# Kernel optimization log

Measured on AMD Instinct MI355X. Metric: run time of the kernel, lower is better.

## Reference

```python
import jax, jax.numpy as jnp
import numpy as np

K = 1024  # codebook size
D = 256   # code dim
B, L = 32, 1024  # batch, tokens


def setup_inputs() -> dict:
    key = jax.random.key(0)
    k1, k2 = jax.random.split(key)
    z_e_x = jax.random.normal(k1, (B, L, D), dtype=jnp.float32)
    # nn.Embedding weight init: uniform(-1/K, 1/K)
    embedding = jax.random.uniform(k2, (K, D), dtype=jnp.float32,
                                   minval=-1.0 / K, maxval=1.0 / K)
    return {"z_e_x": z_e_x, "embedding": embedding}


def reference(z_e_x, embedding):
    # vq(): nearest-neighbor codebook lookup -> integer indices, shape z_e_x.shape[:-1]
    flat = z_e_x.reshape(-1, z_e_x.shape[-1])                      # [N, D]
    # squared L2 distances via expansion: ||z||^2 - 2 z.e + ||e||^2
    d = (jnp.sum(flat * flat, axis=1, keepdims=True)
         - 2.0 * flat @ embedding.T
         + jnp.sum(embedding * embedding, axis=1))                 # [N, K]
    idx = jnp.argmin(d, axis=1)                                    # [N]
    return idx.reshape(z_e_x.shape[:-1])
```

## Files before the change

### kernel.cpp

```cpp
#include <hip/hip_runtime.h>


#define DDIM 256
#define KCODES 1024
#define TAU 1.6e-4f
#define WIN 1.2e-4f
#define LISTCAP 16384
#define CANDCAP 16
#define P2GRID 2048

typedef __attribute__((ext_vector_type(8))) _Float16 f16x8;
typedef __attribute__((ext_vector_type(2))) _Float16 h2;
typedef __attribute__((ext_vector_type(4))) float f32x4;
typedef __attribute__((ext_vector_type(8))) unsigned short u16x8;

__device__ __forceinline__ float block128_sq(const float* __restrict__ a)
{
#pragma clang fp contract(off)
    float r[8];
    #pragma unroll
    for (int j = 0; j < 8; ++j) { float v = a[j]; r[j] = v * v; }
    #pragma unroll
    for (int i = 8; i < 128; i += 8) {
        #pragma unroll
        for (int j = 0; j < 8; ++j) { float v = a[i + j]; r[j] = r[j] + v * v; }
    }
    return ((r[0] + r[1]) + (r[2] + r[3])) + ((r[4] + r[5]) + (r[6] + r[7]));
}

__global__ __launch_bounds__(256) void vq_prep(
    const float* __restrict__ emb, unsigned short* __restrict__ e16,
    float* __restrict__ s2, int* __restrict__ count)
{
    const int tid = threadIdx.x;
    if (blockIdx.x == 0 && tid == 0) *count = 0;

    const int id = blockIdx.x * 256 + tid;
    const float* src = emb + (size_t)id * 8;
    float4 p0 = *reinterpret_cast<const float4*>(src);
    float4 p1 = *reinterpret_cast<const float4*>(src + 4);
    float fv[8] = {p0.x, p0.y, p0.z, p0.w, p1.x, p1.y, p1.z, p1.w};
    u16x8 vh;
    #pragma unroll
    for (int e = 0; e < 8; ++e) {
        _Float16 h = (_Float16)(fv[e] * 1024.0f);
        vh[e] = __builtin_bit_cast(unsigned short, h);
    }
    *reinterpret_cast<u16x8*>(e16 + (size_t)id * 8) = vh;

    if (tid < 8) {
        const int c = blockIdx.x * 8 + tid;
        const float* e = emb + (size_t)c * DDIM;
        s2[c] = block128_sq(e) + block128_sq(e + 128);
    }
}

__global__ __launch_bounds__(256, 2) void vq_pass1(
    const float* __restrict__ z, const unsigned short* __restrict__ e16,
    const float* __restrict__ s2g, int* __restrict__ out,
    int* __restrict__ count, int* __restrict__ list, int N)
{
    __shared__ __align__(16) unsigned short Bt[3][8192];
    __shared__ float s2s[KCODES];
    __shared__ float Lbv[2][64], Lsv[2][64];
    __shared__ int   Lbk[2][64];

    const int tid  = threadIdx.x;
    const int wid  = tid >> 6, lane = tid & 63;
    const int ll   = lane & 15, lg = lane >> 4;
    const int rowHalf  = wid & 1, codeHalf = wid >> 1;
    const int rowbase  = blockIdx.x * 64 + rowHalf * 32;
    const int chbase   = codeHalf * 512;

    for (int c = tid; c < KCODES; c += 256) s2s[c] = s2g[c];

    const int sB     = (ll >> 1) & 3;
    const int rdbase = ll * 32 + ((lg ^ sB) << 3);

    f16x8 afrag[8][2];
    #pragma unroll
    for (int ks = 0; ks < 8; ++ks)
        #pragma unroll
        for (int m = 0; m < 2; ++m) {
            const float* zp = z + (size_t)(rowbase + 16 * m + ll) * DDIM + ks * 32 + lg * 8;
            float4 p0 = *reinterpret_cast<const float4*>(zp);
            float4 p1 = *reinterpret_cast<const float4*>(zp + 4);
            float fv[8] = {p0.x, p0.y, p0.z, p0.w, p1.x, p1.y, p1.z, p1.w};
            #pragma unroll
            for (int e = 0; e < 8; ++e) afrag[ks][m][e] = (_Float16)fv[e];
        }

    #define STAGE(nt_, buf_)                                                      \
        {                                                                         \
            const int nt_v = (nt_);                                               \
            _Pragma("unroll")                                                     \
            for (int q = 0; q < 4; ++q) {                                         \
                int id = q * 256 + tid;                                           \
                int half = id >> 9, rem = id & 511, cl = rem >> 2, pc = rem & 3;  \
                int clog = pc ^ ((cl >> 1) & 3);                                  \
                const unsigned short* src = e16 +                                 \
                    (size_t)(half * 512 + (nt_v >> 3) * 128 + cl) * DDIM          \
                        + (nt_v & 7) * 32 + clog * 8;                             \
                __builtin_amdgcn_global_load_lds(                                 \
                    (const __attribute__((address_space(1))) void*)src,           \
                    (__attribute__((address_space(3))) void*)&Bt[buf_][(size_t)id * 8], \
                    16, 0, 0);                                                    \
            }                                                                     \
        }

    f32x4 acc[2][8];
    float bv[2][4], sv[2][4];
    int   bk[2][4];
    #pragma unroll
    for (int m = 0; m < 2; ++m)
        #pragma unroll
        for (int j = 0; j < 4; ++j) { bv[m][j] = 3.4e38f; sv[m][j] = 3.4e38f; bk[m][j] = 0; }

    STAGE(0, 0);
    STAGE(1, 1);

    for (int ct = 0; ct < 4; ++ct) {
        const f32x4 zero4 = {0.f, 0.f, 0.f, 0.f};
        #pragma unroll
        for (int m = 0; m < 2; ++m)
            #pragma unroll
            for (int n = 0; n < 8; ++n) acc[m][n] = zero4;

        #pragma unroll
        for (int ks = 0; ks < 8; ++ks) {
            const int t = ct * 8 + ks;
            if (t < 31) asm volatile("s_waitcnt vmcnt(4)" ::: "memory");
            else        asm volatile("s_waitcnt vmcnt(0)" ::: "memory");
            __builtin_amdgcn_s_barrier();
            __builtin_amdgcn_sched_barrier(0);

            const unsigned short* bbase = &Bt[t % 3][codeHalf * 4096];
            #pragma unroll
            for (int n = 0; n < 8; ++n) {
                f16x8 bh = *reinterpret_cast<const f16x8*>(bbase + n * 512 + rdbase);
                #pragma unroll
                for (int m = 0; m < 2; ++m)
                    acc[m][n] = __builtin_amdgcn_mfma_f32_16x16x32_f16(
                        afrag[ks][m], bh, acc[m][n], 0, 0, 0);
            }

            if (t + 2 < 32) STAGE(t + 2, (t + 2) % 3);
        }

        #pragma unroll
        for (int n = 0; n < 8; ++n) {
            const int c = chbase + ct * 128 + n * 16 + ll;
            const float s2v = s2s[c];
            #pragma unroll
            for (int m = 0; m < 2; ++m)
                #pragma unroll
                for (int j = 0; j < 4; ++j) {
                    float v = fmaf(-0.001953125f, acc[m][n][j], s2v);
                    if (v < bv[m][j] || (v == bv[m][j] && c < bk[m][j])) {
                        sv[m][j] = bv[m][j]; bv[m][j] = v; bk[m][j] = c;
                    } else {
                        sv[m][j] = fminf(sv[m][j], v);
                    }
                }
        }
    }
    #undef STAGE

    #pragma unroll
    for (int off = 1; off < 16; off <<= 1) {
        #pragma unroll
        for (int m = 0; m < 2; ++m)
            #pragma unroll
            for (int j = 0; j < 4; ++j) {
                float ob = __shfl_xor(bv[m][j], off, 64);
                int   ok = __shfl_xor(bk[m][j], off, 64);
                float os = __shfl_xor(sv[m][j], off, 64);
                if (ob < bv[m][j] || (ob == bv[m][j] && ok < bk[m][j])) {
                    sv[m][j] = fminf(bv[m][j], os); bv[m][j] = ob; bk[m][j] = ok;
                } else {
                    sv[m][j] = fminf(sv[m][j], ob);
                }
            }
    }

    if (ll == 0) {
        #pragma unroll
        for (int m = 0; m < 2; ++m)
            #pragma unroll
            for (int j = 0; j < 4; ++j) {
                int rib = rowHalf * 32 + 16 * m + lg * 4 + j;
                Lbv[codeHalf][rib] = bv[m][j];
                Lsv[codeHalf][rib] = sv[m][j];
                Lbk[codeHalf][rib] = bk[m][j];
            }
    }
    __syncthreads();

    if (tid < 64) {
        const int r = blockIdx.x * 64 + tid;
        if (r < N) {
            float b0 = Lbv[0][tid], s0 = Lsv[0][tid]; int k0 = Lbk[0][tid];
            float b1 = Lbv[1][tid], s1 = Lsv[1][tid]; int k1 = Lbk[1][tid];
            float bb, ss; int kk;
            if (b1 < b0) { bb = b1; kk = k1; ss = fminf(s1, b0); }
            else         { bb = b0; kk = k0; ss = fminf(s0, b1); }
            out[r] = kk;
            if (ss - bb <= TAU) {
                int pos = atomicAdd(count, 1);
                if (pos < LISTCAP) list[pos] = r;
            }
        }
    }
}

__global__ __launch_bounds__(256, 4) void vq_pass2(
    const float* __restrict__ z, const float* __restrict__ emb,
    const unsigned short* __restrict__ e16, const float* __restrict__ s2g,
    const int* __restrict__ count, const int* __restrict__ list,
    int* __restrict__ out)
{
#pragma clang fp contract(off)
    __shared__ __align__(16) float zls[DDIM];
    __shared__ float vls[KCODES];
    __shared__ float s2s[KCODES];
    __shared__ float s1sh, bvsh;
    __shared__ float wmin[4];
    __shared__ int   candc[CANDCAP];
    __shared__ float cand_v[CANDCAP];
    __shared__ int   ncand;

    const int tid  = threadIdx.x;
    const int wv   = tid >> 6, lane = tid & 63;
    const int cslot = lane >> 2;
    const int sub   = lane & 3;

    int cnt = *count; if (cnt > LISTCAP) cnt = LISTCAP;
    if ((int)blockIdx.x >= cnt) return;

    for (int c = tid; c < KCODES; c += 256) s2s[c] = s2g[c];

    for (int idx = blockIdx.x; idx < cnt; idx += P2GRID) {
        const int row = list[idx];

        if (tid < 64)
            *reinterpret_cast<float4*>(&zls[tid * 4]) =
                *reinterpret_cast<const float4*>(z + (size_t)row * DDIM + tid * 4);
        if (tid == 65) ncand = 0;
        __syncthreads();

        if (tid == 0) s1sh = block128_sq(zls) + block128_sq(zls + 128);

        h2 z16[32];
        {
            const float2* zp2 = reinterpret_cast<const float2*>(&zls[0]);
            #pragma unroll
            for (int q = 0; q < 8; ++q)
                #pragma unroll
                for (int j = 0; j < 4; ++j) {
                    float2 f = zp2[q * 16 + sub * 4 + j];
                    h2 a; a[0] = (_Float16)f.x; a[1] = (_Float16)f.y;
                    z16[q * 4 + j] = a;
                }
        }

        #pragma unroll 1
        for (int i = 0; i < 16; ++i) {
            const int c = wv * 256 + i * 16 + cslot;
            const unsigned short* base = e16 + (size_t)c * DDIM;

            float p = 0.f;
            #pragma unroll
            for (int h = 0; h < 2; ++h) {
                f16x8 e0 = *reinterpret_cast<const f16x8*>(base + (4 * h + 0) * 32 + sub * 8);
                f16x8 e1 = *reinterpret_cast<const f16x8*>(base + (4 * h + 1) * 32 + sub * 8);
                f16x8 e2 = *reinterpret_cast<const f16x8*>(base + (4 * h + 2) * 32 + sub * 8);
                f16x8 e3 = *reinterpret_cast<const f16x8*>(base + (4 * h + 3) * 32 + sub * 8);
                #pragma unroll
                for (int j = 0; j < 4; ++j) {
                    h2 a0; a0[0] = e0[2 * j]; a0[1] = e0[2 * j + 1];
                    h2 a1; a1[0] = e1[2 * j]; a1[1] = e1[2 * j + 1];
                    h2 a2; a2[0] = e2[2 * j]; a2[1] = e2[2 * j + 1];
                    h2 a3; a3[0] = e3[2 * j]; a3[1] = e3[2 * j + 1];
#if __has_builtin(__builtin_amdgcn_fdot2)
                    p = __builtin_amdgcn_fdot2(a0, z16[(4 * h + 0) * 4 + j], p, false);
                    p = __builtin_amdgcn_fdot2(a1, z16[(4 * h + 1) * 4 + j], p, false);
                    p = __builtin_amdgcn_fdot2(a2, z16[(4 * h + 2) * 4 + j], p, false);
                    p = __builtin_amdgcn_fdot2(a3, z16[(4 * h + 3) * 4 + j], p, false);
#else
                    p = fmaf((float)a0[0], (float)z16[(4 * h + 0) * 4 + j][0], p);
                    p = fmaf((float)a0[1], (float)z16[(4 * h + 0) * 4 + j][1], p);
                    p = fmaf((float)a1[0], (float)z16[(4 * h + 1) * 4 + j][0], p);
                    p = fmaf((float)a1[1], (float)z16[(4 * h + 1) * 4 + j][1], p);
                    p = fmaf((float)a2[0], (float)z16[(4 * h + 2) * 4 + j][0], p);
                    p = fmaf((float)a2[1], (float)z16[(4 * h + 2) * 4 + j][1], p);
                    p = fmaf((float)a3[0], (float)z16[(4 * h + 3) * 4 + j][0], p);
                    p = fmaf((float)a3[1], (float)z16[(4 * h + 3) * 4 + j][1], p);
#endif
                }
            }
            p += __shfl_xor(p, 1, 64);
            p += __shfl_xor(p, 2, 64);
            if (sub == 0)
                vls[c] = fmaf(-0.001953125f, p, s2s[c]);
        }
        __syncthreads();

        float m = 3.4e38f;
        #pragma unroll
        for (int k = 0; k < 4; ++k) m = fminf(m, vls[tid + 256 * k]);
        #pragma unroll
        for (int off = 1; off < 64; off <<= 1) m = fminf(m, __shfl_xor(m, off, 64));
        if (lane == 0) wmin[wv] = m;
        __syncthreads();
        if (tid == 0)
            bvsh = fminf(fminf(wmin[0], wmin[1]), fminf(wmin[2], wmin[3]));
        __syncthreads();

        const float thr = bvsh + WIN;
        #pragma unroll
        for (int k = 0; k < 4; ++k) {
            int c = tid + 256 * k;
            if (vls[c] <= thr) {
                int p = atomicAdd(&ncand, 1);
                if (p < CANDCAP) candc[p] = c;
            }
        }
        __syncthreads();
        int nc2 = ncand; if (nc2 > CANDCAP) nc2 = CANDCAP;
        const float s1 = s1sh;

        for (int i = wv; i < nc2; i += 4) {
            const int c = candc[i];
            float4 ev4 = *reinterpret_cast<const float4*>(emb + (size_t)c * DDIM + lane * 4);
            const float* zq = &zls[lane * 4];
            double ds = (double)zq[0] * (double)ev4.x;
            ds = fma((double)zq[1], (double)ev4.y, ds);
            ds = fma((double)zq[2], (double)ev4.z, ds);
            ds = fma((double)zq[3], (double)ev4.w, ds);
            #pragma unroll
            for (int off = 1; off < 64; off <<= 1)
                ds += __shfl_xor(ds, off, 64);
            if (lane == 0) {
                float twog = 2.0f * (float)ds;
                float t1   = s1 - twog;
                cand_v[i]  = t1 + s2s[c];
            }
        }
        __syncthreads();

        if (tid == 0) {
            float bb = 3.4e38f; int kb = KCODES - 1;
            for (int i = 0; i < nc2; ++i) {
                float dv = cand_v[i]; int c = candc[i];
                if (dv < bb || (dv == bb && c < kb)) { bb = dv; kb = c; }
            }
            out[row] = kb;
        }
        __syncthreads();
    }
}

extern "C" void kernel_launch(void* const* d_in, const int* in_sizes, int n_in,
                              void* d_out, int out_size, void* d_ws, size_t ws_size,
                              hipStream_t stream) {
    const float* z   = (const float*)d_in[0];
    const float* emb = (const float*)d_in[1];
    int*   out   = (int*)d_out;
    float* s2    = (float*)d_ws;
    int*   count = (int*)((char*)d_ws + 4096);
    int*   list  = (int*)((char*)d_ws + 4224);
    unsigned short* e16 = (unsigned short*)((char*)d_ws + 131072);
    const int N = in_sizes[0] / DDIM;

    vq_prep<<<dim3(128), dim3(256), 0, stream>>>(emb, e16, s2, count);
    vq_pass1<<<dim3(N / 64), dim3(256), 0, stream>>>(z, e16, s2, out, count, list, N);
    vq_pass2<<<dim3(P2GRID), dim3(256), 0, stream>>>(z, emb, e16, s2, count, list, out);
}
```

Before: 74.40 us.

## Restructure VQ pass1 to 128-row blocks with per-wave full-codebook sweep

Pass1 now uses 512-thread blocks covering 128 rows. Each wave owns 16 rows and scans all 1024 codes, instead of splitting code halves across waves and merging them through shared memory. The codebook is staged in 128-code chunks covering the full depth, double-buffered with one barrier per chunk instead of one per 32-wide K slice. This cuts barrier count and drops the cross-wave LDS merge, and each staged B tile is reused by 8 waves. The cost is a larger LDS footprint (128KB of staging), a full vmcnt(0) wait before each chunk, and half the A-fragment reuse per B read.

```diff
diff --git a/kernel.cpp b/kernel.cpp
--- a/kernel.cpp
+++ b/kernel.cpp
@@ -55,52 +55,45 @@
     }
 }
 
-__global__ __launch_bounds__(256, 2) void vq_pass1(
+__global__ __launch_bounds__(512, 2) void vq_pass1(
     const float* __restrict__ z, const unsigned short* __restrict__ e16,
     const float* __restrict__ s2g, int* __restrict__ out,
     int* __restrict__ count, int* __restrict__ list, int N)
 {
-    __shared__ __align__(16) unsigned short Bt[3][8192];
+    __shared__ __align__(16) unsigned short Bt[2][32768];
     __shared__ float s2s[KCODES];
-    __shared__ float Lbv[2][64], Lsv[2][64];
-    __shared__ int   Lbk[2][64];
 
     const int tid  = threadIdx.x;
     const int wid  = tid >> 6, lane = tid & 63;
     const int ll   = lane & 15, lg = lane >> 4;
-    const int rowHalf  = wid & 1, codeHalf = wid >> 1;
-    const int rowbase  = blockIdx.x * 64 + rowHalf * 32;
-    const int chbase   = codeHalf * 512;
-
-    for (int c = tid; c < KCODES; c += 256) s2s[c] = s2g[c];
+    const int rowbase = blockIdx.x * 128 + wid * 16;
+
+    for (int c = tid; c < KCODES; c += 512) s2s[c] = s2g[c];
 
     const int sB     = (ll >> 1) & 3;
     const int rdbase = ll * 32 + ((lg ^ sB) << 3);
 
-    f16x8 afrag[8][2];
-    #pragma unroll
-    for (int ks = 0; ks < 8; ++ks)
-        #pragma unroll
-        for (int m = 0; m < 2; ++m) {
-            const float* zp = z + (size_t)(rowbase + 16 * m + ll) * DDIM + ks * 32 + lg * 8;
-            float4 p0 = *reinterpret_cast<const float4*>(zp);
-            float4 p1 = *reinterpret_cast<const float4*>(zp + 4);
-            float fv[8] = {p0.x, p0.y, p0.z, p0.w, p1.x, p1.y, p1.z, p1.w};
-            #pragma unroll
-            for (int e = 0; e < 8; ++e) afrag[ks][m][e] = (_Float16)fv[e];
-        }
-
-    #define STAGE(nt_, buf_)                                                      \
+    f16x8 afrag[8];
+    #pragma unroll
+    for (int ks = 0; ks < 8; ++ks) {
+        const float* zp = z + (size_t)(rowbase + ll) * DDIM + ks * 32 + lg * 8;
+        float4 p0 = *reinterpret_cast<const float4*>(zp);
+        float4 p1 = *reinterpret_cast<const float4*>(zp + 4);
+        float fv[8] = {p0.x, p0.y, p0.z, p0.w, p1.x, p1.y, p1.z, p1.w};
+        #pragma unroll
+        for (int e = 0; e < 8; ++e) afrag[ks][e] = (_Float16)fv[e];
+    }
+
+    #define STAGE(ct_, buf_)                                                      \
         {                                                                         \
-            const int nt_v = (nt_);                                               \
+            const int ct_v = (ct_);                                               \
             _Pragma("unroll")                                                     \
-            for (int q = 0; q < 4; ++q) {                                         \
-                int id = q * 256 + tid;                                           \
-                int half = id >> 9, rem = id & 511, cl = rem >> 2, pc = rem & 3;  \
+            for (int q = 0; q < 8; ++q) {                                         \
+                int id = q * 512 + tid;                                           \
+                int ks = id >> 9, rem = id & 511, cl = rem >> 2, pc = rem & 3;    \
                 int clog = pc ^ ((cl >> 1) & 3);                                  \
                 const unsigned short* src = e16 +                                 \
-                    (size_t)(half * 512 + (nt_v >> 3) * 128 + cl) * DDIM          \
-                        + (nt_v & 7) * 32 + clog * 8;                             \
+                    (size_t)(ct_v * 128 + cl) * DDIM + ks * 32 + clog * 8;        \
                 __builtin_amdgcn_global_load_lds(                                 \
                     (const __attribute__((address_space(1))) void*)src,           \
                     (__attribute__((address_space(3))) void*)&Bt[buf_][(size_t)id * 8], \
@@ -108,60 +101,50 @@
             }                                                                     \
         }
 
-    f32x4 acc[2][8];
-    float bv[2][4], sv[2][4];
-    int   bk[2][4];
-    #pragma unroll
-    for (int m = 0; m < 2; ++m)
-        #pragma unroll
-        for (int j = 0; j < 4; ++j) { bv[m][j] = 3.4e38f; sv[m][j] = 3.4e38f; bk[m][j] = 0; }
+    float bv[4], sv[4];
+    int   bk[4];
+    #pragma unroll
+    for (int j = 0; j < 4; ++j) { bv[j] = 3.4e38f; sv[j] = 3.4e38f; bk[j] = 0; }
 
     STAGE(0, 0);
-    STAGE(1, 1);
-
-    for (int ct = 0; ct < 4; ++ct) {
+
+    for (int ct = 0; ct < 8; ++ct) {
+        const int buf = ct & 1;
+        asm volatile("s_waitcnt vmcnt(0)" ::: "memory");
+        __builtin_amdgcn_s_barrier();
+        __builtin_amdgcn_sched_barrier(0);
+
+        if (ct < 7) STAGE(ct + 1, buf ^ 1);
+
+        f32x4 acc[8];
         const f32x4 zero4 = {0.f, 0.f, 0.f, 0.f};
         #pragma unroll
-        for (int m = 0; m < 2; ++m)
-            #pragma unroll
-            for (int n = 0; n < 8; ++n) acc[m][n] = zero4;
+        for (int n = 0; n < 8; ++n) acc[n] = zero4;
 
         #pragma unroll
         for (int ks = 0; ks < 8; ++ks) {
-            const int t = ct * 8 + ks;
-            if (t < 31) asm volatile("s_waitcnt vmcnt(4)" ::: "memory");
-            else        asm volatile("s_waitcnt vmcnt(0)" ::: "memory");
-            __builtin_amdgcn_s_barrier();
-            __builtin_amdgcn_sched_barrier(0);
-
-            const unsigned short* bbase = &Bt[t % 3][codeHalf * 4096];
             #pragma unroll
             for (int n = 0; n < 8; ++n) {
-                f16x8 bh = *reinterpret_cast<const f16x8*>(bbase + n * 512 + rdbase);
-                #pragma unroll
-                for (int m = 0; m < 2; ++m)
-                    acc[m][n] = __builtin_amdgcn_mfma_f32_16x16x32_f16(
-                        afrag[ks][m], bh, acc[m][n], 0, 0, 0);
-            }
-
-            if (t + 2 < 32) STAGE(t + 2, (t + 2) % 3);
+                f16x8 bh = *reinterpret_cast<const f16x8*>(
+                    &Bt[buf][ks * 4096 + n * 512 + rdbase]);
+                acc[n] = __builtin_amdgcn_mfma_f32_16x16x32_f16(
+                    afrag[ks], bh, acc[n], 0, 0, 0);
+            }
         }
 
         #pragma unroll
         for (int n = 0; n < 8; ++n) {
-            const int c = chbase + ct * 128 + n * 16 + ll;
+            const int c = ct * 128 + n * 16 + ll;
             const float s2v = s2s[c];
             #pragma unroll
-            for (int m = 0; m < 2; ++m)
-                #pragma unroll
-                for (int j = 0; j < 4; ++j) {
-                    float v = fmaf(-0.001953125f, acc[m][n][j], s2v);
-                    if (v < bv[m][j] || (v == bv[m][j] && c < bk[m][j])) {
-                        sv[m][j] = bv[m][j]; bv[m][j] = v; bk[m][j] = c;
-                    } else {
-                        sv[m][j] = fminf(sv[m][j], v);
-                    }
+            for (int j = 0; j < 4; ++j) {
+                float v = fmaf(-0.001953125f, acc[n][j], s2v);
+                if (v < bv[j] || (v == bv[j] && c < bk[j])) {
+                    sv[j] = bv[j]; bv[j] = v; bk[j] = c;
+                } else {
+                    sv[j] = fminf(sv[j], v);
                 }
+            }
         }
     }
     #undef STAGE
@@ -169,45 +152,28 @@
     #pragma unroll
     for (int off = 1; off < 16; off <<= 1) {
         #pragma unroll
-        for (int m = 0; m < 2; ++m)
-            #pragma unroll
-            for (int j = 0; j < 4; ++j) {
-                float ob = __shfl_xor(bv[m][j], off, 64);
-                int   ok = __shfl_xor(bk[m][j], off, 64);
-                float os = __shfl_xor(sv[m][j], off, 64);
-                if (ob < bv[m][j] || (ob == bv[m][j] && ok < bk[m][j])) {
-                    sv[m][j] = fminf(bv[m][j], os); bv[m][j] = ob; bk[m][j] = ok;
-                } else {
-                    sv[m][j] = fminf(sv[m][j], ob);
+        for (int j = 0; j < 4; ++j) {
+            float ob = __shfl_xor(bv[j], off, 64);
+            int   ok = __shfl_xor(bk[j], off, 64);
+            float os = __shfl_xor(sv[j], off, 64);
+            if (ob < bv[j] || (ob == bv[j] && ok < bk[j])) {
+                sv[j] = fminf(bv[j], os); bv[j] = ob; bk[j] = ok;
+            } else {
+                sv[j] = fminf(sv[j], ob);
+            }
+        }
+    }
+
+    if (ll == 0) {
+        #pragma unroll
+        for (int j = 0; j < 4; ++j) {
+            int r = rowbase + lg * 4 + j;
+            if (r < N) {
+                out[r] = bk[j];
+                if (sv[j] - bv[j] <= TAU) {
+                    int pos = atomicAdd(count, 1);
+                    if (pos < LISTCAP) list[pos] = r;
                 }
-            }
-    }
-
-    if (ll == 0) {
-        #pragma unroll
-        for (int m = 0; m < 2; ++m)
-            #pragma unroll
-            for (int j = 0; j < 4; ++j) {
-                int rib = rowHalf * 32 + 16 * m + lg * 4 + j;
-                Lbv[codeHalf][rib] = bv[m][j];
-                Lsv[codeHalf][rib] = sv[m][j];
-                Lbk[codeHalf][rib] = bk[m][j];
-            }
-    }
-    __syncthreads();
-
-    if (tid < 64) {
-        const int r = blockIdx.x * 64 + tid;
-        if (r < N) {
-            float b0 = Lbv[0][tid], s0 = Lsv[0][tid]; int k0 = Lbk[0][tid];
-            float b1 = Lbv[1][tid], s1 = Lsv[1][tid]; int k1 = Lbk[1][tid];
-            float bb, ss; int kk;
-            if (b1 < b0) { bb = b1; kk = k1; ss = fminf(s1, b0); }
-            else         { bb = b0; kk = k0; ss = fminf(s0, b1); }
-            out[r] = kk;
-            if (ss - bb <= TAU) {
-                int pos = atomicAdd(count, 1);
-                if (pos < LISTCAP) list[pos] = r;
             }
         }
     }
@@ -373,6 +339,6 @@
     const int N = in_sizes[0] / DDIM;
 
     vq_prep<<<dim3(128), dim3(256), 0, stream>>>(emb, e16, s2, count);
-    vq_pass1<<<dim3(N / 64), dim3(256), 0, stream>>>(z, e16, s2, out, count, list, N);
+    vq_pass1<<<dim3(N / 128), dim3(512), 0, stream>>>(z, e16, s2, out, count, list, N);
     vq_pass2<<<dim3(P2GRID), dim3(256), 0, stream>>>(z, emb, e16, s2, count, list, out);
 }
```

After: 72.89 us. 2.0% less time.

## Process 128 rows per block with full-K code tiles and double buffering

Applied to the files above, without the earlier changes.

Pass1 now gives each wave 32 rows against all 1024 codes instead of splitting codes between wave pairs. Each stage loads a whole 128-code by 256-dim fp16 tile (64 KB per buffer, double-buffered), so there is one barrier per 128-code tile instead of one per k-slice. This also removes the cross-wave LDS merge of the two code halves. Codebook reuse per block doubles, but LDS use rises to about 132 KB, occupancy drops to one block per CU with half as many blocks, and the fetch of each tile is waited on fully before compute.

```diff
diff --git a/kernel.cpp b/kernel.cpp
--- a/kernel.cpp
+++ b/kernel.cpp
@@ -55,29 +55,44 @@
     }
 }
 
-__global__ __launch_bounds__(256, 2) void vq_pass1(
+__global__ __launch_bounds__(256, 1) void vq_pass1(
     const float* __restrict__ z, const unsigned short* __restrict__ e16,
     const float* __restrict__ s2g, int* __restrict__ out,
     int* __restrict__ count, int* __restrict__ list, int N)
 {
-    __shared__ __align__(16) unsigned short Bt[3][8192];
+    __shared__ __align__(16) unsigned short Bt[2][32768];
     __shared__ float s2s[KCODES];
-    __shared__ float Lbv[2][64], Lsv[2][64];
-    __shared__ int   Lbk[2][64];
 
     const int tid  = threadIdx.x;
     const int wid  = tid >> 6, lane = tid & 63;
     const int ll   = lane & 15, lg = lane >> 4;
-    const int rowHalf  = wid & 1, codeHalf = wid >> 1;
-    const int rowbase  = blockIdx.x * 64 + rowHalf * 32;
-    const int chbase   = codeHalf * 512;
-
-    for (int c = tid; c < KCODES; c += 256) s2s[c] = s2g[c];
+    const int rowbase = blockIdx.x * 128 + wid * 32;
 
     const int sB     = (ll >> 1) & 3;
     const int rdbase = ll * 32 + ((lg ^ sB) << 3);
 
-    f16x8 afrag[8][2];
+    #define STAGE(ct_, buf_)                                                      \
+        {                                                                         \
+            const int ct_v = (ct_);                                               \
+            _Pragma("unroll")                                                     \
+            for (int q = 0; q < 16; ++q) {                                        \
+                int id = q * 256 + tid;                                           \
+                int ks = id >> 9, rem = id & 511, cl = rem >> 2, pc = rem & 3;    \
+                int clog = pc ^ ((cl >> 1) & 3);                                  \
+                const unsigned short* src = e16 +                                 \
+                    (size_t)(ct_v * 128 + cl) * DDIM + ks * 32 + clog * 8;        \
+                __builtin_amdgcn_global_load_lds(                                 \
+                    (const __attribute__((address_space(1))) void*)src,           \
+                    (__attribute__((address_space(3))) void*)&Bt[buf_][(size_t)id * 8], \
+                    16, 0, 0);                                                    \
+            }                                                                     \
+        }
+
+    STAGE(0, 0);
+
+    for (int c = tid; c < KCODES; c += 256) s2s[c] = s2g[c];
+
+    f16x8 afrag[2][8];
     #pragma unroll
     for (int ks = 0; ks < 8; ++ks)
         #pragma unroll
@@ -87,28 +102,9 @@
             float4 p1 = *reinterpret_cast<const float4*>(zp + 4);
             float fv[8] = {p0.x, p0.y, p0.z, p0.w, p1.x, p1.y, p1.z, p1.w};
             #pragma unroll
-            for (int e = 0; e < 8; ++e) afrag[ks][m][e] = (_Float16)fv[e];
-        }
-
-    #define STAGE(nt_, buf_)                                                      \
-        {                                                                         \
-            const int nt_v = (nt_);                                               \
-            _Pragma("unroll")                                                     \
-            for (int q = 0; q < 4; ++q) {                                         \
-                int id = q * 256 + tid;                                           \
-                int half = id >> 9, rem = id & 511, cl = rem >> 2, pc = rem & 3;  \
-                int clog = pc ^ ((cl >> 1) & 3);                                  \
-                const unsigned short* src = e16 +                                 \
-                    (size_t)(half * 512 + (nt_v >> 3) * 128 + cl) * DDIM          \
-                        + (nt_v & 7) * 32 + clog * 8;                             \
-                __builtin_amdgcn_global_load_lds(                                 \
-                    (const __attribute__((address_space(1))) void*)src,           \
-                    (__attribute__((address_space(3))) void*)&Bt[buf_][(size_t)id * 8], \
-                    16, 0, 0);                                                    \
-            }                                                                     \
-        }
-
-    f32x4 acc[2][8];
+            for (int e = 0; e < 8; ++e) afrag[m][ks][e] = (_Float16)fv[e];
+        }
+
     float bv[2][4], sv[2][4];
     int   bk[2][4];
     #pragma unroll
@@ -116,10 +112,15 @@
         #pragma unroll
         for (int j = 0; j < 4; ++j) { bv[m][j] = 3.4e38f; sv[m][j] = 3.4e38f; bk[m][j] = 0; }
 
-    STAGE(0, 0);
-    STAGE(1, 1);
-
-    for (int ct = 0; ct < 4; ++ct) {
+    for (int ct = 0; ct < 8; ++ct) {
+        const int buf = ct & 1;
+        asm volatile("s_waitcnt vmcnt(0)" ::: "memory");
+        __builtin_amdgcn_s_barrier();
+        __builtin_amdgcn_sched_barrier(0);
+
+        if (ct < 7) STAGE(ct + 1, buf ^ 1);
+
+        f32x4 acc[2][8];
         const f32x4 zero4 = {0.f, 0.f, 0.f, 0.f};
         #pragma unroll
         for (int m = 0; m < 2; ++m)
@@ -128,28 +129,20 @@
 
         #pragma unroll
         for (int ks = 0; ks < 8; ++ks) {
-            const int t = ct * 8 + ks;
-            if (t < 31) asm volatile("s_waitcnt vmcnt(4)" ::: "memory");
-            else        asm volatile("s_waitcnt vmcnt(0)" ::: "memory");
-            __builtin_amdgcn_s_barrier();
-            __builtin_amdgcn_sched_barrier(0);
-
-            const unsigned short* bbase = &Bt[t % 3][codeHalf * 4096];
             #pragma unroll
             for (int n = 0; n < 8; ++n) {
-                f16x8 bh = *reinterpret_cast<const f16x8*>(bbase + n * 512 + rdbase);
+                f16x8 bh = *reinterpret_cast<const f16x8*>(
+                    &Bt[buf][ks * 4096 + n * 512 + rdbase]);
                 #pragma unroll
                 for (int m = 0; m < 2; ++m)
                     acc[m][n] = __builtin_amdgcn_mfma_f32_16x16x32_f16(
-                        afrag[ks][m], bh, acc[m][n], 0, 0, 0);
-            }
-
-            if (t + 2 < 32) STAGE(t + 2, (t + 2) % 3);
+                        afrag[m][ks], bh, acc[m][n], 0, 0, 0);
+            }
         }
 
         #pragma unroll
         for (int n = 0; n < 8; ++n) {
-            const int c = chbase + ct * 128 + n * 16 + ll;
+            const int c = ct * 128 + n * 16 + ll;
             const float s2v = s2s[c];
             #pragma unroll
             for (int m = 0; m < 2; ++m)
@@ -188,28 +181,15 @@
         for (int m = 0; m < 2; ++m)
             #pragma unroll
             for (int j = 0; j < 4; ++j) {
-                int rib = rowHalf * 32 + 16 * m + lg * 4 + j;
-                Lbv[codeHalf][rib] = bv[m][j];
-                Lsv[codeHalf][rib] = sv[m][j];
-                Lbk[codeHalf][rib] = bk[m][j];
-            }
-    }
-    __syncthreads();
-
-    if (tid < 64) {
-        const int r = blockIdx.x * 64 + tid;
-        if (r < N) {
-            float b0 = Lbv[0][tid], s0 = Lsv[0][tid]; int k0 = Lbk[0][tid];
-            float b1 = Lbv[1][tid], s1 = Lsv[1][tid]; int k1 = Lbk[1][tid];
-            float bb, ss; int kk;
-            if (b1 < b0) { bb = b1; kk = k1; ss = fminf(s1, b0); }
-            else         { bb = b0; kk = k0; ss = fminf(s0, b1); }
-            out[r] = kk;
-            if (ss - bb <= TAU) {
-                int pos = atomicAdd(count, 1);
-                if (pos < LISTCAP) list[pos] = r;
-            }
-        }
+                int r = rowbase + 16 * m + lg * 4 + j;
+                if (r < N) {
+                    out[r] = bk[m][j];
+                    if (sv[m][j] - bv[m][j] <= TAU) {
+                        int pos = atomicAdd(count, 1);
+                        if (pos < LISTCAP) list[pos] = r;
+                    }
+                }
+            }
     }
 }
 
@@ -373,6 +353,6 @@
     const int N = in_sizes[0] / DDIM;
 
     vq_prep<<<dim3(128), dim3(256), 0, stream>>>(emb, e16, s2, count);
-    vq_pass1<<<dim3(N / 64), dim3(256), 0, stream>>>(z, e16, s2, out, count, list, N);
+    vq_pass1<<<dim3(N / 128), dim3(256), 0, stream>>>(z, e16, s2, out, count, list, N);
     vq_pass2<<<dim3(P2GRID), dim3(256), 0, stream>>>(z, emb, e16, s2, count, list, out);
 }
```

New measurement: 96.23 us. 1.29x slower.
